# Kernel optimization log

Hardware: AMD Instinct MI355X
Metric: run time of the kernel (lower is better)

## Reference

```python
import jax, jax.numpy as jnp
import numpy as np

N_NODES = 100000
N_EDGES = 1600000
F = 64          # node_features (in == out for EvolveGCNO)
HID = 64        # hidden_size


def setup_inputs() -> dict:
    key = jax.random.key(0)
    ks = jax.random.split(key, 12)
    s = 1.0 / np.sqrt(F)
    inp = {
        "x": jax.random.normal(ks[0], (N_NODES, F), dtype=jnp.float32),
        "edge_index": jax.random.randint(ks[1], (2, N_EDGES), 0, N_NODES, dtype=jnp.int64),
        "edge_weight": jax.random.uniform(ks[2], (N_EDGES,), dtype=jnp.float32),
        # evolving GCN weight (initial_weight of EvolveGCNO)
        "W0": jax.random.uniform(ks[3], (F, F), jnp.float32, -s, s),
        # GRU (input_size=F, hidden_size=F): gates ordered r, z, n
        "gru_Wi": jax.random.uniform(ks[4], (3 * F, F), jnp.float32, -s, s),
        "gru_Wh": jax.random.uniform(ks[5], (3 * F, F), jnp.float32, -s, s),
        "gru_bi": jax.random.uniform(ks[6], (3 * F,), jnp.float32, -s, s),
        "gru_bh": jax.random.uniform(ks[7], (3 * F,), jnp.float32, -s, s),
        # projection F -> HID and head HID -> 1
        "proj_W": jax.random.uniform(ks[8], (HID, F), jnp.float32, -s, s),
        "proj_b": jax.random.uniform(ks[9], (HID,), jnp.float32, -s, s),
        "lin_W": jax.random.uniform(ks[10], (1, HID), jnp.float32, -1.0 / np.sqrt(HID), 1.0 / np.sqrt(HID)),
        "lin_b": jax.random.uniform(ks[11], (1,), jnp.float32, -1.0 / np.sqrt(HID), 1.0 / np.sqrt(HID)),
    }
    return inp


def reference(x, edge_index, edge_weight, W0, gru_Wi, gru_Wh, gru_bi, gru_bh,
              proj_W, proj_b, lin_W, lin_b):
    N = x.shape[0]
    # --- EvolveGCNO weight evolution: one GRU step, rows of W0 are both input and hidden ---
    gi = W0 @ gru_Wi.T + gru_bi  # [F, 3F]
    gh = W0 @ gru_Wh.T + gru_bh  # [F, 3F]
    i_r, i_z, i_n = jnp.split(gi, 3, axis=1)
    h_r, h_z, h_n = jnp.split(gh, 3, axis=1)
    r = jax.nn.sigmoid(i_r + h_r)
    z = jax.nn.sigmoid(i_z + h_z)
    n = jnp.tanh(i_n + r * h_n)
    W = (1.0 - z) * n + z * W0  # evolved GCN weight [F, F]

    # --- GCNConv with fixed evolved W: X' = D^-1/2 (A + I) D^-1/2 (X W) ---
    xw = x @ W  # [N, F]
    src, dst = edge_index[0], edge_index[1]
    loop = jnp.arange(N)
    src2 = jnp.concatenate([src, loop])
    dst2 = jnp.concatenate([dst, loop])
    w2 = jnp.concatenate([edge_weight, jnp.ones((N,), xw.dtype)])  # self-loop weight 1
    deg = jax.ops.segment_sum(w2, dst2, num_segments=N)
    dinv = jnp.where(deg > 0, jax.lax.rsqrt(deg), 0.0)
    norm = dinv[src2] * w2 * dinv[dst2]  # [E + N]
    h = jax.ops.segment_sum(xw[src2] * norm[:, None], dst2, num_segments=N)  # [N, F]

    # --- MLP head (dropout is identity in eval) ---
    h = jax.nn.relu(h @ proj_W.T + proj_b)
    return h @ lin_W.T + lin_b  # [N, 1]
```

## Files before the change

kernel.cpp:

```cpp
#include <hip/hip_runtime.h>
#include <stdint.h>

#define FDIM 64
#define BINSH 6
#define NBINS 1563
#define BCAP 1536
#define OVCAP 8192
#define PSTAGE 8192
#define PBLK 196
#define LSTRIDE 72

__device__ __forceinline__ float bf2f(unsigned int u) {
    union { float f; uint32_t i; } v; v.i = (u & 0xFFFFu) << 16; return v.f;
}
__device__ __forceinline__ unsigned short f2bf(float f) {
    union { float f; uint32_t i; } v; v.f = f;
    uint32_t u = v.i;
    u += 0x7FFFu + ((u >> 16) & 1u);
    return (unsigned short)(u >> 16);
}

__global__ __launch_bounds__(256) void k_sentinel(float* out, int N, float val) {
    int n = blockIdx.x * 256 + threadIdx.x;
    if (n < N) out[n] = (n == 0) ? val : 0.f;
}

__global__ __launch_bounds__(1024) void k_prep(
    const int* __restrict__ src, const int* __restrict__ dst,
    const float* __restrict__ ew, int* __restrict__ gcnt,
    int2* __restrict__ part, int* __restrict__ ovf_cnt,
    int* __restrict__ ovs, int* __restrict__ ovd, float* __restrict__ ovw, int E,
    const float* __restrict__ W0, const float* __restrict__ Wi,
    const float* __restrict__ Wh, const float* __restrict__ bi,
    const float* __restrict__ bh, const float* __restrict__ projW,
    float* __restrict__ M) {
    __shared__ char sm[12504];
    int t = threadIdx.x;
    if (blockIdx.x < PBLK) {
        int* hist = (int*)sm;
        int* lcur = hist + NBINS;
        for (int b = t; b < NBINS; b += 1024) hist[b] = 0;
        __syncthreads();
        int e0 = blockIdx.x * PSTAGE;
        int cnt = E - e0; if (cnt > PSTAGE) cnt = PSTAGE;
        for (int i = t; i < cnt; i += 1024) atomicAdd(&hist[dst[e0 + i] >> BINSH], 1);
        __syncthreads();
        for (int b = t; b < NBINS; b += 1024) {
            int h = hist[b];
            lcur[b] = h ? atomicAdd(&gcnt[b], h) : 0;
        }
        __syncthreads();
        for (int i = t; i < cnt; i += 1024) {
            int e = e0 + i;
            int d = dst[e];
            int b = d >> BINSH;
            int p = atomicAdd(&lcur[b], 1);
            if (p < BCAP) {
                part[(size_t)b * BCAP + p] = make_int2(src[e] | ((d & 63) << 20),
                                                       __float_as_int(ew[e]));
            } else {
                int op = atomicAdd(ovf_cnt, 1);
                if (op < OVCAP) {
                    ovs[op] = src[e];
                    ovd[op] = d;
                    ovw[op] = ew[e];
                }
            }
        }
    } else {
        int i = blockIdx.x - PBLK;
        float* w0s  = (float*)sm;
        float* wrow = w0s + 64;
        if (t < 64) w0s[t] = W0[i * 64 + t];
        __syncthreads();
        if (t < 64) {
            int j = t;
            float a0 = 0.f, a1 = 0.f, a2 = 0.f, b0 = 0.f, b1 = 0.f, b2 = 0.f;
#pragma unroll 8
            for (int k = 0; k < 64; k++) {
                float w0k = w0s[k];
                a0 += w0k * Wi[(j)       * 64 + k];
                a1 += w0k * Wi[(64 + j)  * 64 + k];
                a2 += w0k * Wi[(128 + j) * 64 + k];
                b0 += w0k * Wh[(j)       * 64 + k];
                b1 += w0k * Wh[(64 + j)  * 64 + k];
                b2 += w0k * Wh[(128 + j) * 64 + k];
            }
            float ir = a0 + bi[j],        hr = b0 + bh[j];
            float iz = a1 + bi[64 + j],   hz = b1 + bh[64 + j];
            float in_ = a2 + bi[128 + j], hn = b2 + bh[128 + j];
            float r = 1.f / (1.f + expf(-(ir + hr)));
            float z = 1.f / (1.f + expf(-(iz + hz)));
            float n = tanhf(in_ + r * hn);
            wrow[j] = (1.f - z) * n + z * w0s[j];
        }
        __syncthreads();
        if (t < 64) {
            float s = 0.f;
#pragma unroll 8
            for (int q = 0; q < 64; q++) s += wrow[q] * projW[t * 64 + q];
            M[i * 64 + t] = s;
        }
    }
}

__global__ __launch_bounds__(256) void k_deg(
    const int* __restrict__ gcnt, const int2* __restrict__ part,
    const int* __restrict__ ovf_cnt, const int* __restrict__ ovd,
    const float* __restrict__ ovw, float* __restrict__ dinv,
    int* __restrict__ loffg, int N) {
    __shared__ float dl[64];
    __shared__ int   cntl[64];
    __shared__ int   lofl[65];
    int t = threadIdx.x, b = blockIdx.x;
    if (t < 64) { dl[t] = 1.0f; cntl[t] = 0; }
    __syncthreads();
    int c = gcnt[b]; if (c > BCAP) c = BCAP;
    const int2* pe = part + (size_t)b * BCAP;
    for (int i = t; i < c; i += 256) {
        int2 e = pe[i];
        int nl = (e.x >> 20) & 63;
        atomicAdd(&dl[nl], __int_as_float(e.y));
        atomicAdd(&cntl[nl], 1);
    }
    int m = *ovf_cnt; if (m > OVCAP) m = OVCAP;
    for (int i = t; i < m; i += 256) {
        int d = ovd[i];
        if ((d >> BINSH) == b) atomicAdd(&dl[d & 63], ovw[i]);
    }
    __syncthreads();
    if (t == 0) {
        int o = 0;
#pragma unroll 16
        for (int k = 0; k < 64; k++) { lofl[k] = o; o += cntl[k]; }
        lofl[64] = o;
    }
    __syncthreads();
    if (t < 64) {
        int n = b * 64 + t;
        if (n < N) dinv[n] = rsqrtf(dl[t]);
    }
    if (t < 65) loffg[b * LSTRIDE + t] = lofl[t];
}

__global__ __launch_bounds__(256) void k_xm(
    const float* __restrict__ x, const float* __restrict__ M,
    unsigned short* __restrict__ xm, int N,
    const float* __restrict__ dinv) {
    __shared__ char sm[34816];
    int t = threadIdx.x;
    float* xs = (float*)sm;
    float* ms = xs + 64 * 68;
    int nb = blockIdx.x * 64;
#pragma unroll
    for (int i = 0; i < 4; i++) {
        int lin = i * 1024 + t * 4;
        int row = lin >> 6, col = lin & 63;
        int node = nb + row;
        float4 v = make_float4(0.f, 0.f, 0.f, 0.f);
        if (node < N) v = *(const float4*)(x + (size_t)node * 64 + col);
        *(float4*)&xs[row * 68 + col] = v;
        *(float4*)&ms[row * 68 + col] = *(const float4*)(M + lin);
    }
    __syncthreads();
    int tj = t & 15, tn = t >> 4;
    float acc[4][4] = {};
    for (int k = 0; k < 64; k += 4) {
        float4 xv[4], mv[4];
#pragma unroll
        for (int nn = 0; nn < 4; nn++) xv[nn] = *(const float4*)&xs[(tn * 4 + nn) * 68 + k];
#pragma unroll
        for (int kk = 0; kk < 4; kk++) mv[kk] = *(const float4*)&ms[(k + kk) * 68 + tj * 4];
#pragma unroll
        for (int nn = 0; nn < 4; nn++) {
            const float* xp = (const float*)&xv[nn];
#pragma unroll
            for (int kk = 0; kk < 4; kk++) {
                float xk = xp[kk];
                const float* mp = (const float*)&mv[kk];
                acc[nn][0] += xk * mp[0];
                acc[nn][1] += xk * mp[1];
                acc[nn][2] += xk * mp[2];
                acc[nn][3] += xk * mp[3];
            }
        }
    }
#pragma unroll
    for (int nn = 0; nn < 4; nn++) {
        int node = nb + tn * 4 + nn;
        if (node < N) {
            float dr = dinv[node];
            ushort4 o;
            o.x = f2bf(acc[nn][0] * dr); o.y = f2bf(acc[nn][1] * dr);
            o.z = f2bf(acc[nn][2] * dr); o.w = f2bf(acc[nn][3] * dr);
            *(ushort4*)&xm[(size_t)node * 64 + tj * 4] = o;
        }
    }
}

__global__ __launch_bounds__(256) void k_gf(
    const unsigned short* __restrict__ xm, const float* __restrict__ dinv,
    const int* __restrict__ gcnt, const int2* __restrict__ part,
    const int* __restrict__ loffg,
    const float* __restrict__ projB, const float* __restrict__ linW,
    const float* __restrict__ linB, const int* __restrict__ ovf_cnt,
    const int* __restrict__ ovs, const int* __restrict__ ovd,
    const float* __restrict__ ovw, float* __restrict__ out, int N) {
    __shared__ int  loff[65];
    __shared__ int  lcur[64];
    __shared__ int2 ledge[BCAP];
    __shared__ float pbs[64], lws[64];
    int t = threadIdx.x, b = blockIdx.x;
    if (t < 65) loff[t] = loffg[b * LSTRIDE + t];
    if (t < 64) { pbs[t] = projB[t]; lws[t] = linW[t]; }
    __syncthreads();
    if (t < 64) lcur[t] = loff[t];
    __syncthreads();
    int c = gcnt[b]; if (c > BCAP) c = BCAP;
    const int2* pe = part + (size_t)b * BCAP;
    for (int i = t; i < c; i += 256) {
        int2 e = pe[i];
        int p = atomicAdd(&lcur[(e.x >> 20) & 63], 1);
        ledge[p] = e;
    }
    __syncthreads();
    int m = *ovf_cnt; if (m > OVCAP) m = OVCAP;
    float lb = linB[0];
    int wv = t >> 6, lane = t & 63, eg = lane >> 4, fq = lane & 15, f = fq * 4;
    for (int nl = wv; nl < 64; nl += 4) {
        int n = b * 64 + nl;
        if (n >= N) continue;
        float dn = dinv[n];
        int beg = loff[nl], end = loff[nl + 1];
        float a0 = 0.f, a1 = 0.f, a2 = 0.f, a3 = 0.f;
        float b0 = 0.f, b1 = 0.f, b2 = 0.f, b3 = 0.f;
        float c0 = 0.f, c1 = 0.f, c2 = 0.f, c3 = 0.f;
        float d0 = 0.f, d1 = 0.f, d2 = 0.f, d3 = 0.f;
        int i = beg + eg;
        for (; i + 12 < end; i += 16) {
            int2 e0 = ledge[i];
            int2 e1 = ledge[i + 4];
            int2 e2 = ledge[i + 8];
            int2 e3 = ledge[i + 12];
            uint2 u0 = *(const uint2*)&xm[(size_t)(e0.x & 0xFFFFF) * 64 + f];
            uint2 u1 = *(const uint2*)&xm[(size_t)(e1.x & 0xFFFFF) * 64 + f];
            uint2 u2 = *(const uint2*)&xm[(size_t)(e2.x & 0xFFFFF) * 64 + f];
            uint2 u3 = *(const uint2*)&xm[(size_t)(e3.x & 0xFFFFF) * 64 + f];
            float w0 = __int_as_float(e0.y);
            float w1 = __int_as_float(e1.y);
            float w2 = __int_as_float(e2.y);
            float w3 = __int_as_float(e3.y);
            a0 += w0 * bf2f(u0.x); a1 += w0 * bf2f(u0.x >> 16);
            a2 += w0 * bf2f(u0.y); a3 += w0 * bf2f(u0.y >> 16);
            b0 += w1 * bf2f(u1.x); b1 += w1 * bf2f(u1.x >> 16);
            b2 += w1 * bf2f(u1.y); b3 += w1 * bf2f(u1.y >> 16);
            c0 += w2 * bf2f(u2.x); c1 += w2 * bf2f(u2.x >> 16);
            c2 += w2 * bf2f(u2.y); c3 += w2 * bf2f(u2.y >> 16);
            d0 += w3 * bf2f(u3.x); d1 += w3 * bf2f(u3.x >> 16);
            d2 += w3 * bf2f(u3.y); d3 += w3 * bf2f(u3.y >> 16);
        }
        for (; i + 4 < end; i += 8) {
            int2 e0 = ledge[i];
            int2 e1 = ledge[i + 4];
            uint2 u0 = *(const uint2*)&xm[(size_t)(e0.x & 0xFFFFF) * 64 + f];
            uint2 u1 = *(const uint2*)&xm[(size_t)(e1.x & 0xFFFFF) * 64 + f];
            float w0 = __int_as_float(e0.y);
            float w1 = __int_as_float(e1.y);
            a0 += w0 * bf2f(u0.x); a1 += w0 * bf2f(u0.x >> 16);
            a2 += w0 * bf2f(u0.y); a3 += w0 * bf2f(u0.y >> 16);
            b0 += w1 * bf2f(u1.x); b1 += w1 * bf2f(u1.x >> 16);
            b2 += w1 * bf2f(u1.y); b3 += w1 * bf2f(u1.y >> 16);
        }
        for (; i < end; i += 4) {
            int2 e0 = ledge[i];
            uint2 u0 = *(const uint2*)&xm[(size_t)(e0.x & 0xFFFFF) * 64 + f];
            float w0 = __int_as_float(e0.y);
            a0 += w0 * bf2f(u0.x); a1 += w0 * bf2f(u0.x >> 16);
            a2 += w0 * bf2f(u0.y); a3 += w0 * bf2f(u0.y >> 16);
        }
        a0 += b0 + c0 + d0; a1 += b1 + c1 + d1;
        a2 += b2 + c2 + d2; a3 += b3 + c3 + d3;
        a0 *= dn; a1 *= dn; a2 *= dn; a3 *= dn;
        a0 += __shfl_xor(a0, 16); a1 += __shfl_xor(a1, 16);
        a2 += __shfl_xor(a2, 16); a3 += __shfl_xor(a3, 16);
        a0 += __shfl_xor(a0, 32); a1 += __shfl_xor(a1, 32);
        a2 += __shfl_xor(a2, 32); a3 += __shfl_xor(a3, 32);
        if (eg == 0) {
            {
                uint2 u = *(const uint2*)&xm[(size_t)n * 64 + f];
                a0 += dn * bf2f(u.x); a1 += dn * bf2f(u.x >> 16);
                a2 += dn * bf2f(u.y); a3 += dn * bf2f(u.y >> 16);
            }
            for (int q = 0; q < m; q++) {
                if (ovd[q] == n) {
                    int s = ovs[q];
                    float nm = ovw[q] * dn;
                    uint2 u = *(const uint2*)&xm[(size_t)s * 64 + f];
                    a0 += nm * bf2f(u.x); a1 += nm * bf2f(u.x >> 16);
                    a2 += nm * bf2f(u.y); a3 += nm * bf2f(u.y >> 16);
                }
            }
            float v0 = a0 + pbs[f],     v1 = a1 + pbs[f + 1];
            float v2 = a2 + pbs[f + 2], v3 = a3 + pbs[f + 3];
            float s = (v0 > 0.f ? v0 : 0.f) * lws[f]
                    + (v1 > 0.f ? v1 : 0.f) * lws[f + 1]
                    + (v2 > 0.f ? v2 : 0.f) * lws[f + 2]
                    + (v3 > 0.f ? v3 : 0.f) * lws[f + 3];
            s += __shfl_xor(s, 1); s += __shfl_xor(s, 2);
            s += __shfl_xor(s, 4); s += __shfl_xor(s, 8);
            if (fq == 0) out[n] = s + lb;
        }
    }
}

extern "C" void kernel_launch(void* const* d_in, const int* in_sizes, int n_in,
                              void* d_out, int out_size, void* d_ws, size_t ws_size,
                              hipStream_t stream) {
    const float* x   = (const float*)d_in[0];
    const int*   ei  = (const int*)d_in[1];
    const float* ew  = (const float*)d_in[2];
    const float* W0  = (const float*)d_in[3];
    const float* gWi = (const float*)d_in[4];
    const float* gWh = (const float*)d_in[5];
    const float* gbi = (const float*)d_in[6];
    const float* gbh = (const float*)d_in[7];
    const float* pW  = (const float*)d_in[8];
    const float* pb  = (const float*)d_in[9];
    const float* lW  = (const float*)d_in[10];
    const float* lb  = (const float*)d_in[11];
    float* out = (float*)d_out;

    static const int EXPSZ[12] = {6400000, 3200000, 1600000, 4096, 12288, 12288,
                                  192, 192, 4096, 64, 64, 1};
    int mism = -1;
    for (int i = 0; i < 12 && i < n_in; i++)
        if (in_sizes[i] != EXPSZ[i]) { mism = i; break; }
    if (mism >= 0) {
        k_sentinel<<<(out_size + 255) / 256, 256, 0, stream>>>(out, out_size,
                                                               ldexpf(1.f, 30 + 3 * mism));
        return;
    }

    int N = in_sizes[0] / FDIM;
    int E = in_sizes[1] / 2;
    const int* src = ei;
    const int* dst = ei + E;

    char* wsb = (char*)d_ws;
    float* M       = (float*)(wsb);
    int*   gcnt    = (int*)  (wsb + (32u << 10));
    int*   ovf_cnt = (int*)  (wsb + (39u << 10));
    int*   ovs     = (int*)  (wsb + (44u << 10));
    int*   ovd     = (int*)  (wsb + (76u << 10));
    float* ovw     = (float*)(wsb + (108u << 10));
    float* dinv    = (float*)(wsb + (1u << 20));
    int*   loffg   = (int*)  (wsb + 1572864u);
    int2*  part    = (int2*) (wsb + (2u << 20));
    unsigned short* xm = (unsigned short*)(wsb + (22u << 20));

    hipMemsetAsync(gcnt, 0, (8u << 10), stream);

    k_prep<<<PBLK + 64, 1024, 0, stream>>>(src, dst, ew, gcnt, part,
                                           ovf_cnt, ovs, ovd, ovw, E,
                                           W0, gWi, gWh, gbi, gbh, pW, M);
    k_deg<<<NBINS, 256, 0, stream>>>(gcnt, part, ovf_cnt, ovd, ovw,
                                     dinv, loffg, N);
    k_xm<<<NBINS, 256, 0, stream>>>(x, M, xm, N, dinv);
    k_gf<<<NBINS, 256, 0, stream>>>(xm, dinv, gcnt, part, loffg, pb, lW, lb,
                                    ovf_cnt, ovs, ovd, ovw, out, N);
}
```

Baseline: 193.3 us.

## Sort edges locally in prep and fuse degree pass with XM matmul

k_prep now sorts each stage's edges by bin in shared memory using a block prefix scan, then writes them to the global partitions in sorted order so the scattered stores become more contiguous. The source-side dinv scaling is moved out of the XM kernel and into the gather kernel, applied per edge weight, with the self-loop scaled by dinv squared. Because XM no longer needs dinv, the degree and XM kernels are merged into a single launch whose blocks split between the two tasks and run concurrently. The cost is much more shared memory per prep block (about 100KB) and an extra dinv gather per edge in k_gf.

```diff
diff --git a/kernel.cpp b/kernel.cpp
--- a/kernel.cpp
+++ b/kernel.cpp
@@ -34,11 +34,15 @@
     const float* __restrict__ Wh, const float* __restrict__ bi,
     const float* __restrict__ bh, const float* __restrict__ projW,
     float* __restrict__ M) {
-    __shared__ char sm[12504];
+    __shared__ int2 sorted_[PSTAGE];
+    __shared__ int  gposa[PSTAGE];
+    __shared__ int  hist[NBINS];
+    __shared__ int  lbase[NBINS];
+    __shared__ int  lcur[NBINS];
+    __shared__ int  gboff[NBINS];
+    __shared__ int  wsum[16];
     int t = threadIdx.x;
     if (blockIdx.x < PBLK) {
-        int* hist = (int*)sm;
-        int* lcur = hist + NBINS;
         for (int b = t; b < NBINS; b += 1024) hist[b] = 0;
         __syncthreads();
         int e0 = blockIdx.x * PSTAGE;
@@ -47,29 +51,59 @@
         __syncthreads();
         for (int b = t; b < NBINS; b += 1024) {
             int h = hist[b];
-            lcur[b] = h ? atomicAdd(&gcnt[b], h) : 0;
-        }
+            gboff[b] = h ? atomicAdd(&gcnt[b], h) : 0;
+        }
+        int b0i = 2 * t, b1i = 2 * t + 1;
+        int h0 = (b0i < NBINS) ? hist[b0i] : 0;
+        int h1 = (b1i < NBINS) ? hist[b1i] : 0;
+        int c2 = h0 + h1;
+        int lane = t & 63, wid = t >> 6;
+        int v = c2;
+#pragma unroll
+        for (int d = 1; d < 64; d <<= 1) {
+            int o = __shfl_up(v, d);
+            if (lane >= d) v += o;
+        }
+        if (lane == 63) wsum[wid] = v;
+        __syncthreads();
+        if (t < 16) {
+            int w = wsum[t];
+#pragma unroll
+            for (int d = 1; d < 16; d <<= 1) {
+                int o = __shfl_up(w, d);
+                if (t >= d) w += o;
+            }
+            wsum[t] = w;
+        }
+        __syncthreads();
+        int base = (wid > 0) ? wsum[wid - 1] : 0;
+        int excl = base + v - c2;
+        if (b0i < NBINS) { lbase[b0i] = excl;      lcur[b0i] = excl; }
+        if (b1i < NBINS) { lbase[b1i] = excl + h0; lcur[b1i] = excl + h0; }
         __syncthreads();
         for (int i = t; i < cnt; i += 1024) {
             int e = e0 + i;
             int d = dst[e];
             int b = d >> BINSH;
             int p = atomicAdd(&lcur[b], 1);
-            if (p < BCAP) {
-                part[(size_t)b * BCAP + p] = make_int2(src[e] | ((d & 63) << 20),
-                                                       __float_as_int(ew[e]));
+            sorted_[p] = make_int2(src[e] | ((d & 63) << 20), __float_as_int(ew[e]));
+            int off = gboff[b] + (p - lbase[b]);
+            if (off < BCAP) {
+                gposa[p] = b * BCAP + off;
             } else {
+                gposa[p] = -1;
                 int op = atomicAdd(ovf_cnt, 1);
-                if (op < OVCAP) {
-                    ovs[op] = src[e];
-                    ovd[op] = d;
-                    ovw[op] = ew[e];
-                }
-            }
+                if (op < OVCAP) { ovs[op] = src[e]; ovd[op] = d; ovw[op] = ew[e]; }
+            }
+        }
+        __syncthreads();
+        for (int j = t; j < cnt; j += 1024) {
+            int g = gposa[j];
+            if (g >= 0) part[g] = sorted_[j];
         }
     } else {
         int i = blockIdx.x - PBLK;
-        float* w0s  = (float*)sm;
+        float* w0s  = (float*)sorted_;
         float* wrow = w0s + 64;
         if (t < 64) w0s[t] = W0[i * 64 + t];
         __syncthreads();
@@ -104,97 +138,95 @@
     }
 }
 
-__global__ __launch_bounds__(256) void k_deg(
+__global__ __launch_bounds__(256) void k_xmdeg(
+    const float* __restrict__ x, const float* __restrict__ M,
+    unsigned short* __restrict__ xm, int N,
     const int* __restrict__ gcnt, const int2* __restrict__ part,
     const int* __restrict__ ovf_cnt, const int* __restrict__ ovd,
     const float* __restrict__ ovw, float* __restrict__ dinv,
-    int* __restrict__ loffg, int N) {
-    __shared__ float dl[64];
-    __shared__ int   cntl[64];
-    __shared__ int   lofl[65];
-    int t = threadIdx.x, b = blockIdx.x;
-    if (t < 64) { dl[t] = 1.0f; cntl[t] = 0; }
-    __syncthreads();
-    int c = gcnt[b]; if (c > BCAP) c = BCAP;
-    const int2* pe = part + (size_t)b * BCAP;
-    for (int i = t; i < c; i += 256) {
-        int2 e = pe[i];
-        int nl = (e.x >> 20) & 63;
-        atomicAdd(&dl[nl], __int_as_float(e.y));
-        atomicAdd(&cntl[nl], 1);
-    }
-    int m = *ovf_cnt; if (m > OVCAP) m = OVCAP;
-    for (int i = t; i < m; i += 256) {
-        int d = ovd[i];
-        if ((d >> BINSH) == b) atomicAdd(&dl[d & 63], ovw[i]);
-    }
-    __syncthreads();
-    if (t == 0) {
-        int o = 0;
-#pragma unroll 16
-        for (int k = 0; k < 64; k++) { lofl[k] = o; o += cntl[k]; }
-        lofl[64] = o;
-    }
-    __syncthreads();
-    if (t < 64) {
-        int n = b * 64 + t;
-        if (n < N) dinv[n] = rsqrtf(dl[t]);
-    }
-    if (t < 65) loffg[b * LSTRIDE + t] = lofl[t];
-}
-
-__global__ __launch_bounds__(256) void k_xm(
-    const float* __restrict__ x, const float* __restrict__ M,
-    unsigned short* __restrict__ xm, int N,
-    const float* __restrict__ dinv) {
+    int* __restrict__ loffg) {
     __shared__ char sm[34816];
     int t = threadIdx.x;
-    float* xs = (float*)sm;
-    float* ms = xs + 64 * 68;
-    int nb = blockIdx.x * 64;
-#pragma unroll
-    for (int i = 0; i < 4; i++) {
-        int lin = i * 1024 + t * 4;
-        int row = lin >> 6, col = lin & 63;
-        int node = nb + row;
-        float4 v = make_float4(0.f, 0.f, 0.f, 0.f);
-        if (node < N) v = *(const float4*)(x + (size_t)node * 64 + col);
-        *(float4*)&xs[row * 68 + col] = v;
-        *(float4*)&ms[row * 68 + col] = *(const float4*)(M + lin);
-    }
-    __syncthreads();
-    int tj = t & 15, tn = t >> 4;
-    float acc[4][4] = {};
-    for (int k = 0; k < 64; k += 4) {
-        float4 xv[4], mv[4];
-#pragma unroll
-        for (int nn = 0; nn < 4; nn++) xv[nn] = *(const float4*)&xs[(tn * 4 + nn) * 68 + k];
-#pragma unroll
-        for (int kk = 0; kk < 4; kk++) mv[kk] = *(const float4*)&ms[(k + kk) * 68 + tj * 4];
+    if (blockIdx.x < NBINS) {
+        float* xs = (float*)sm;
+        float* ms = xs + 64 * 68;
+        int nb = blockIdx.x * 64;
+#pragma unroll
+        for (int i = 0; i < 4; i++) {
+            int lin = i * 1024 + t * 4;
+            int row = lin >> 6, col = lin & 63;
+            int node = nb + row;
+            float4 v = make_float4(0.f, 0.f, 0.f, 0.f);
+            if (node < N) v = *(const float4*)(x + (size_t)node * 64 + col);
+            *(float4*)&xs[row * 68 + col] = v;
+            *(float4*)&ms[row * 68 + col] = *(const float4*)(M + lin);
+        }
+        __syncthreads();
+        int tj = t & 15, tn = t >> 4;
+        float acc[4][4] = {};
+        for (int k = 0; k < 64; k += 4) {
+            float4 xv[4], mv[4];
+#pragma unroll
+            for (int nn = 0; nn < 4; nn++) xv[nn] = *(const float4*)&xs[(tn * 4 + nn) * 68 + k];
+#pragma unroll
+            for (int kk = 0; kk < 4; kk++) mv[kk] = *(const float4*)&ms[(k + kk) * 68 + tj * 4];
+#pragma unroll
+            for (int nn = 0; nn < 4; nn++) {
+                const float* xp = (const float*)&xv[nn];
+#pragma unroll
+                for (int kk = 0; kk < 4; kk++) {
+                    float xk = xp[kk];
+                    const float* mp = (const float*)&mv[kk];
+                    acc[nn][0] += xk * mp[0];
+                    acc[nn][1] += xk * mp[1];
+                    acc[nn][2] += xk * mp[2];
+                    acc[nn][3] += xk * mp[3];
+                }
+            }
+        }
 #pragma unroll
         for (int nn = 0; nn < 4; nn++) {
-            const float* xp = (const float*)&xv[nn];
-#pragma unroll
-            for (int kk = 0; kk < 4; kk++) {
-                float xk = xp[kk];
-                const float* mp = (const float*)&mv[kk];
-                acc[nn][0] += xk * mp[0];
-                acc[nn][1] += xk * mp[1];
-                acc[nn][2] += xk * mp[2];
-                acc[nn][3] += xk * mp[3];
-            }
-        }
-    }
-#pragma unroll
-    for (int nn = 0; nn < 4; nn++) {
-        int node = nb + tn * 4 + nn;
-        if (node < N) {
-            float dr = dinv[node];
-            ushort4 o;
-            o.x = f2bf(acc[nn][0] * dr); o.y = f2bf(acc[nn][1] * dr);
-            o.z = f2bf(acc[nn][2] * dr); o.w = f2bf(acc[nn][3] * dr);
-            *(ushort4*)&xm[(size_t)node * 64 + tj * 4] = o;
-        }
+            int node = nb + tn * 4 + nn;
+            if (node < N) {
+                ushort4 o;
+                o.x = f2bf(acc[nn][0]); o.y = f2bf(acc[nn][1]);
+                o.z = f2bf(acc[nn][2]); o.w = f2bf(acc[nn][3]);
+                *(ushort4*)&xm[(size_t)node * 64 + tj * 4] = o;
+            }
+        }
+    } else {
+        int b = blockIdx.x - NBINS;
+        float* dl   = (float*)sm;
+        int*   cntl = (int*)(dl + 64);
+        int*   lofl = cntl + 64;
+        if (t < 64) { dl[t] = 1.0f; cntl[t] = 0; }
+        __syncthreads();
+        int c = gcnt[b]; if (c > BCAP) c = BCAP;
+        const int2* pe = part + (size_t)b * BCAP;
+        for (int i = t; i < c; i += 256) {
+            int2 e = pe[i];
+            int nl = (e.x >> 20) & 63;
+            atomicAdd(&dl[nl], __int_as_float(e.y));
+            atomicAdd(&cntl[nl], 1);
+        }
+        int m = *ovf_cnt; if (m > OVCAP) m = OVCAP;
+        for (int i = t; i < m; i += 256) {
+            int d = ovd[i];
+            if ((d >> BINSH) == b) atomicAdd(&dl[d & 63], ovw[i]);
+        }
+        __syncthreads();
+        if (t == 0) {
+            int o = 0;
+#pragma unroll 16
+            for (int k = 0; k < 64; k++) { lofl[k] = o; o += cntl[k]; }
+            lofl[64] = o;
+        }
+        __syncthreads();
+        if (t < 64) {
+            int n = b * 64 + t;
+            if (n < N) dinv[n] = rsqrtf(dl[t]);
+        }
+        if (t < 65) loffg[b * LSTRIDE + t] = lofl[t];
     }
 }
 
@@ -220,8 +252,10 @@
     const int2* pe = part + (size_t)b * BCAP;
     for (int i = t; i < c; i += 256) {
         int2 e = pe[i];
+        int s = e.x & 0xFFFFF;
+        float nw = dinv[s] * __int_as_float(e.y);
         int p = atomicAdd(&lcur[(e.x >> 20) & 63], 1);
-        ledge[p] = e;
+        ledge[p] = make_int2(e.x, __float_as_int(nw));
     }
     __syncthreads();
     int m = *ovf_cnt; if (m > OVCAP) m = OVCAP;
@@ -288,13 +322,14 @@
         if (eg == 0) {
             {
                 uint2 u = *(const uint2*)&xm[(size_t)n * 64 + f];
-                a0 += dn * bf2f(u.x); a1 += dn * bf2f(u.x >> 16);
-                a2 += dn * bf2f(u.y); a3 += dn * bf2f(u.y >> 16);
+                float sl = dn * dn;
+                a0 += sl * bf2f(u.x); a1 += sl * bf2f(u.x >> 16);
+                a2 += sl * bf2f(u.y); a3 += sl * bf2f(u.y >> 16);
             }
             for (int q = 0; q < m; q++) {
                 if (ovd[q] == n) {
                     int s = ovs[q];
-                    float nm = ovw[q] * dn;
+                    float nm = dinv[s] * ovw[q] * dn;
                     uint2 u = *(const uint2*)&xm[(size_t)s * 64 + f];
                     a0 += nm * bf2f(u.x); a1 += nm * bf2f(u.x >> 16);
                     a2 += nm * bf2f(u.y); a3 += nm * bf2f(u.y >> 16);
@@ -363,9 +398,8 @@
     k_prep<<<PBLK + 64, 1024, 0, stream>>>(src, dst, ew, gcnt, part,
                                            ovf_cnt, ovs, ovd, ovw, E,
                                            W0, gWi, gWh, gbi, gbh, pW, M);
-    k_deg<<<NBINS, 256, 0, stream>>>(gcnt, part, ovf_cnt, ovd, ovw,
-                                     dinv, loffg, N);
-    k_xm<<<NBINS, 256, 0, stream>>>(x, M, xm, N, dinv);
+    k_xmdeg<<<NBINS * 2, 256, 0, stream>>>(x, M, xm, N, gcnt, part,
+                                           ovf_cnt, ovd, ovw, dinv, loffg);
     k_gf<<<NBINS, 256, 0, stream>>>(xm, dinv, gcnt, part, loffg, pb, lW, lb,
                                     ovf_cnt, ovs, ovd, ovw, out, N);
 }
```

New measurement: 188.6 us, median of 2. 2.4% less time.

## Merge degree and XM kernels into one launch, move source norm into gather

Applied to the files above, without the earlier changes.

The degree/offset kernel and the X·M projection kernel become one launch, with even blocks doing the projection and odd blocks doing the degree work. Since xm no longer depends on dinv, the source-side normalisation moves into k_gf, which folds dinv[src] into each edge weight while staging edges into LDS. The self-loop and overflow edges are adjusted to match. k_gf now runs 512 threads (8 waves) per block, and the prep kernel uses twice as many blocks with half the stage size, at the cost of an extra random dinv read per edge.

```diff
diff --git a/kernel.cpp b/kernel.cpp
--- a/kernel.cpp
+++ b/kernel.cpp
@@ -6,8 +6,8 @@
 #define NBINS 1563
 #define BCAP 1536
 #define OVCAP 8192
-#define PSTAGE 8192
-#define PBLK 196
+#define PSTAGE 4096
+#define PBLK 392
 #define LSTRIDE 72
 
 __device__ __forceinline__ float bf2f(unsigned int u) {
@@ -104,101 +104,99 @@
     }
 }
 
-__global__ __launch_bounds__(256) void k_deg(
+__global__ __launch_bounds__(256) void k_xmdeg(
+    const float* __restrict__ x, const float* __restrict__ M,
+    unsigned short* __restrict__ xm, int N,
     const int* __restrict__ gcnt, const int2* __restrict__ part,
     const int* __restrict__ ovf_cnt, const int* __restrict__ ovd,
     const float* __restrict__ ovw, float* __restrict__ dinv,
-    int* __restrict__ loffg, int N) {
-    __shared__ float dl[64];
-    __shared__ int   cntl[64];
-    __shared__ int   lofl[65];
-    int t = threadIdx.x, b = blockIdx.x;
-    if (t < 64) { dl[t] = 1.0f; cntl[t] = 0; }
-    __syncthreads();
-    int c = gcnt[b]; if (c > BCAP) c = BCAP;
-    const int2* pe = part + (size_t)b * BCAP;
-    for (int i = t; i < c; i += 256) {
-        int2 e = pe[i];
-        int nl = (e.x >> 20) & 63;
-        atomicAdd(&dl[nl], __int_as_float(e.y));
-        atomicAdd(&cntl[nl], 1);
-    }
-    int m = *ovf_cnt; if (m > OVCAP) m = OVCAP;
-    for (int i = t; i < m; i += 256) {
-        int d = ovd[i];
-        if ((d >> BINSH) == b) atomicAdd(&dl[d & 63], ovw[i]);
-    }
-    __syncthreads();
-    if (t == 0) {
-        int o = 0;
-#pragma unroll 16
-        for (int k = 0; k < 64; k++) { lofl[k] = o; o += cntl[k]; }
-        lofl[64] = o;
-    }
-    __syncthreads();
-    if (t < 64) {
-        int n = b * 64 + t;
-        if (n < N) dinv[n] = rsqrtf(dl[t]);
-    }
-    if (t < 65) loffg[b * LSTRIDE + t] = lofl[t];
-}
-
-__global__ __launch_bounds__(256) void k_xm(
-    const float* __restrict__ x, const float* __restrict__ M,
-    unsigned short* __restrict__ xm, int N,
-    const float* __restrict__ dinv) {
+    int* __restrict__ loffg) {
     __shared__ char sm[34816];
     int t = threadIdx.x;
-    float* xs = (float*)sm;
-    float* ms = xs + 64 * 68;
-    int nb = blockIdx.x * 64;
-#pragma unroll
-    for (int i = 0; i < 4; i++) {
-        int lin = i * 1024 + t * 4;
-        int row = lin >> 6, col = lin & 63;
-        int node = nb + row;
-        float4 v = make_float4(0.f, 0.f, 0.f, 0.f);
-        if (node < N) v = *(const float4*)(x + (size_t)node * 64 + col);
-        *(float4*)&xs[row * 68 + col] = v;
-        *(float4*)&ms[row * 68 + col] = *(const float4*)(M + lin);
-    }
-    __syncthreads();
-    int tj = t & 15, tn = t >> 4;
-    float acc[4][4] = {};
-    for (int k = 0; k < 64; k += 4) {
-        float4 xv[4], mv[4];
-#pragma unroll
-        for (int nn = 0; nn < 4; nn++) xv[nn] = *(const float4*)&xs[(tn * 4 + nn) * 68 + k];
-#pragma unroll
-        for (int kk = 0; kk < 4; kk++) mv[kk] = *(const float4*)&ms[(k + kk) * 68 + tj * 4];
+    if ((blockIdx.x & 1) == 0) {
+        float* xs = (float*)sm;
+        float* ms = xs + 64 * 68;
+        int nb = (blockIdx.x >> 1) * 64;
+#pragma unroll
+        for (int i = 0; i < 4; i++) {
+            int lin = i * 1024 + t * 4;
+            int row = lin >> 6, col = lin & 63;
+            int node = nb + row;
+            float4 v = make_float4(0.f, 0.f, 0.f, 0.f);
+            if (node < N) v = *(const float4*)(x + (size_t)node * 64 + col);
+            *(float4*)&xs[row * 68 + col] = v;
+            *(float4*)&ms[row * 68 + col] = *(const float4*)(M + lin);
+        }
+        __syncthreads();
+        int tj = t & 15, tn = t >> 4;
+        float acc[4][4] = {};
+        for (int k = 0; k < 64; k += 4) {
+            float4 xv[4], mv[4];
+#pragma unroll
+            for (int nn = 0; nn < 4; nn++) xv[nn] = *(const float4*)&xs[(tn * 4 + nn) * 68 + k];
+#pragma unroll
+            for (int kk = 0; kk < 4; kk++) mv[kk] = *(const float4*)&ms[(k + kk) * 68 + tj * 4];
+#pragma unroll
+            for (int nn = 0; nn < 4; nn++) {
+                const float* xp = (const float*)&xv[nn];
+#pragma unroll
+                for (int kk = 0; kk < 4; kk++) {
+                    float xk = xp[kk];
+                    const float* mp = (const float*)&mv[kk];
+                    acc[nn][0] += xk * mp[0];
+                    acc[nn][1] += xk * mp[1];
+                    acc[nn][2] += xk * mp[2];
+                    acc[nn][3] += xk * mp[3];
+                }
+            }
+        }
 #pragma unroll
         for (int nn = 0; nn < 4; nn++) {
-            const float* xp = (const float*)&xv[nn];
-#pragma unroll
-            for (int kk = 0; kk < 4; kk++) {
-                float xk = xp[kk];
-                const float* mp = (const float*)&mv[kk];
-                acc[nn][0] += xk * mp[0];
-                acc[nn][1] += xk * mp[1];
-                acc[nn][2] += xk * mp[2];
-                acc[nn][3] += xk * mp[3];
-            }
-        }
-    }
-#pragma unroll
-    for (int nn = 0; nn < 4; nn++) {
-        int node = nb + tn * 4 + nn;
-        if (node < N) {
-            float dr = dinv[node];
-            ushort4 o;
-            o.x = f2bf(acc[nn][0] * dr); o.y = f2bf(acc[nn][1] * dr);
-            o.z = f2bf(acc[nn][2] * dr); o.w = f2bf(acc[nn][3] * dr);
-            *(ushort4*)&xm[(size_t)node * 64 + tj * 4] = o;
-        }
-    }
-}
-
-__global__ __launch_bounds__(256) void k_gf(
+            int node = nb + tn * 4 + nn;
+            if (node < N) {
+                ushort4 o;
+                o.x = f2bf(acc[nn][0]); o.y = f2bf(acc[nn][1]);
+                o.z = f2bf(acc[nn][2]); o.w = f2bf(acc[nn][3]);
+                *(ushort4*)&xm[(size_t)node * 64 + tj * 4] = o;
+            }
+        }
+    } else {
+        int b = blockIdx.x >> 1;
+        float* dl   = (float*)sm;
+        int*   cntl = (int*)(dl + 64);
+        int*   lofl = cntl + 64;
+        if (t < 64) { dl[t] = 1.0f; cntl[t] = 0; }
+        __syncthreads();
+        int c = gcnt[b]; if (c > BCAP) c = BCAP;
+        const int2* pe = part + (size_t)b * BCAP;
+        for (int i = t; i < c; i += 256) {
+            int2 e = pe[i];
+            int nl = (e.x >> 20) & 63;
+            atomicAdd(&dl[nl], __int_as_float(e.y));
+            atomicAdd(&cntl[nl], 1);
+        }
+        int m = *ovf_cnt; if (m > OVCAP) m = OVCAP;
+        for (int i = t; i < m; i += 256) {
+            int d = ovd[i];
+            if ((d >> BINSH) == b) atomicAdd(&dl[d & 63], ovw[i]);
+        }
+        __syncthreads();
+        if (t == 0) {
+            int o = 0;
+#pragma unroll 16
+            for (int k = 0; k < 64; k++) { lofl[k] = o; o += cntl[k]; }
+            lofl[64] = o;
+        }
+        __syncthreads();
+        if (t < 64) {
+            int n = b * 64 + t;
+            if (n < N) dinv[n] = rsqrtf(dl[t]);
+        }
+        if (t < 65) loffg[b * LSTRIDE + t] = lofl[t];
+    }
+}
+
+__global__ __launch_bounds__(512) void k_gf(
     const unsigned short* __restrict__ xm, const float* __restrict__ dinv,
     const int* __restrict__ gcnt, const int2* __restrict__ part,
     const int* __restrict__ loffg,
@@ -218,16 +216,18 @@
     __syncthreads();
     int c = gcnt[b]; if (c > BCAP) c = BCAP;
     const int2* pe = part + (size_t)b * BCAP;
-    for (int i = t; i < c; i += 256) {
+    for (int i = t; i < c; i += 512) {
         int2 e = pe[i];
+        int s = e.x & 0xFFFFF;
+        float nw = dinv[s] * __int_as_float(e.y);
         int p = atomicAdd(&lcur[(e.x >> 20) & 63], 1);
-        ledge[p] = e;
+        ledge[p] = make_int2(e.x, __float_as_int(nw));
     }
     __syncthreads();
     int m = *ovf_cnt; if (m > OVCAP) m = OVCAP;
     float lb = linB[0];
     int wv = t >> 6, lane = t & 63, eg = lane >> 4, fq = lane & 15, f = fq * 4;
-    for (int nl = wv; nl < 64; nl += 4) {
+    for (int nl = wv; nl < 64; nl += 8) {
         int n = b * 64 + nl;
         if (n >= N) continue;
         float dn = dinv[n];
@@ -288,13 +288,14 @@
         if (eg == 0) {
             {
                 uint2 u = *(const uint2*)&xm[(size_t)n * 64 + f];
-                a0 += dn * bf2f(u.x); a1 += dn * bf2f(u.x >> 16);
-                a2 += dn * bf2f(u.y); a3 += dn * bf2f(u.y >> 16);
+                float sl = dn * dn;
+                a0 += sl * bf2f(u.x); a1 += sl * bf2f(u.x >> 16);
+                a2 += sl * bf2f(u.y); a3 += sl * bf2f(u.y >> 16);
             }
             for (int q = 0; q < m; q++) {
                 if (ovd[q] == n) {
                     int s = ovs[q];
-                    float nm = ovw[q] * dn;
+                    float nm = dinv[s] * ovw[q] * dn;
                     uint2 u = *(const uint2*)&xm[(size_t)s * 64 + f];
                     a0 += nm * bf2f(u.x); a1 += nm * bf2f(u.x >> 16);
                     a2 += nm * bf2f(u.y); a3 += nm * bf2f(u.y >> 16);
@@ -363,9 +364,8 @@
     k_prep<<<PBLK + 64, 1024, 0, stream>>>(src, dst, ew, gcnt, part,
                                            ovf_cnt, ovs, ovd, ovw, E,
                                            W0, gWi, gWh, gbi, gbh, pW, M);
-    k_deg<<<NBINS, 256, 0, stream>>>(gcnt, part, ovf_cnt, ovd, ovw,
-                                     dinv, loffg, N);
-    k_xm<<<NBINS, 256, 0, stream>>>(x, M, xm, N, dinv);
-    k_gf<<<NBINS, 256, 0, stream>>>(xm, dinv, gcnt, part, loffg, pb, lW, lb,
+    k_xmdeg<<<NBINS * 2, 256, 0, stream>>>(x, M, xm, N, gcnt, part,
+                                           ovf_cnt, ovd, ovw, dinv, loffg);
+    k_gf<<<NBINS, 512, 0, stream>>>(xm, dinv, gcnt, part, loffg, pb, lW, lb,
                                     ovf_cnt, ovs, ovd, ovw, out, N);
 }
```

Result: no change. 192.4 us (-0.5%).
